# Performance work log

Hardware: AMD Instinct MI355X
Metric: run time of the kernel (lower is better)

## Reference

```python
import jax, jax.numpy as jnp
import numpy as np

B, F, D = 4096, 39, 16          # batch, num_field, embedding_size
V = 1000000                     # num_feat (vocab)
H1, H2 = 128, 128               # cin_layer_sizes
INPUT_DIM = F * D               # 624
FC_DIM = H1 // 2 + H2           # 192 (split_half)
DEEP = [400, 400]
BN_EPS = 1e-5


def setup_inputs() -> dict:
    key = jax.random.key(0)
    ks = jax.random.split(key, 16)
    xav = lambda k, shp: jax.random.normal(k, shp, jnp.float32) * np.sqrt(2.0 / (shp[0] + shp[-1]))
    return {
        "feat_index": jax.random.randint(ks[0], (B, F), 0, V),
        "feat_value": jax.random.uniform(ks[1], (B, F), jnp.float32),
        "emb_table": xav(ks[2], (V, D)),
        "linear_w": xav(ks[3], (INPUT_DIM, 1)),
        "linear_b": jnp.zeros((1,), jnp.float32),
        "conv_w1": xav(ks[4], (H1, F, F)),          # (out, h_prev, m) == conv1d 1x1 weight reshaped
        "conv_b1": jnp.zeros((H1,), jnp.float32),
        "conv_w2": xav(ks[5], (H2, H1 // 2, F)),
        "conv_b2": jnp.zeros((H2,), jnp.float32),
        "deep_w1": xav(ks[6], (INPUT_DIM, DEEP[0])),
        "deep_b1": jnp.zeros((DEEP[0],), jnp.float32),
        "bn_g1": jnp.ones((DEEP[0],), jnp.float32),
        "bn_b1": jnp.zeros((DEEP[0],), jnp.float32),
        "deep_w2": xav(ks[7], (DEEP[0], DEEP[1])),
        "deep_b2": jnp.zeros((DEEP[1],), jnp.float32),
        "bn_g2": jnp.ones((DEEP[1],), jnp.float32),
        "bn_b2": jnpp if False else jnp.zeros((DEEP[1],), jnp.float32),
        "out_w": xav(ks[8], (1 + FC_DIM + DEEP[1], 1)),
        "out_b": jnp.zeros((1,), jnp.float32),
    }


def _bn(x, g, b):
    # torch BatchNorm1d in training mode: biased batch variance
    m = x.mean(axis=0)
    v = x.var(axis=0)
    return g * (x - m) * jax.lax.rsqrt(v + BN_EPS) + b


def reference(feat_index, feat_value, emb_table, linear_w, linear_b,
              conv_w1, conv_b1, conv_w2, conv_b2,
              deep_w1, deep_b1, bn_g1, bn_b1,
              deep_w2, deep_b2, bn_g2, bn_b2,
              out_w, out_b):
    e = emb_table[feat_index]                      # [B, F, D]
    flat = e.reshape(e.shape[0], -1)               # [B, F*D]
    linear_part = flat @ linear_w + linear_b       # [B, 1]

    # CIN: fused outer-product + 1x1 conv (x_k[b,o,d] = sum_{h,m} W[o,h,m] x_prev[b,h,d] x0[b,m,d])
    x0 = e
    h1 = jax.nn.relu(jnp.einsum('bhd,bmd,ohm->bod', x0, x0, conv_w1) + conv_b1[None, :, None])
    nxt, hi1 = jnp.split(h1, 2, axis=1)            # split_half
    h2 = jax.nn.relu(jnp.einsum('bhd,bmd,ohm->bod', nxt, x0, conv_w2) + conv_b2[None, :, None])
    res = jnp.concatenate([hi1, h2], axis=1).sum(axis=2)   # [B, FC_DIM]

    # Deep tower (dropout off / deterministic)
    y = jax.nn.relu(_bn(flat @ deep_w1 + deep_b1, bn_g1, bn_b1))
    y = jax.nn.relu(_bn(y @ deep_w2 + deep_b2, bn_g2, bn_b2))

    cat = jnp.concatenate([linear_part, res, y], axis=1)   # [B, 593]
    return cat @ out_w + out_b
```

## Files before the change

kernel.cpp:

```cpp
#include <hip/hip_runtime.h>

#define BATCH   4096
#define NF      39
#define ED      16
#define IN_DIM  624
#define DW      400
#define BN_EPS  1e-5f
#define NKSG    78
#define AK1     640
#define NKS1    20
#define NKS2    13
#define WCOL    416

typedef __attribute__((ext_vector_type(8))) short short8;
typedef __attribute__((ext_vector_type(4))) float f32x4;
typedef __attribute__((ext_vector_type(2))) float f32x2;
typedef unsigned short u16;

__device__ inline unsigned pack_hi2(float a, float b) {
  return __builtin_amdgcn_perm(__float_as_uint(b), __float_as_uint(a), 0x07060302u);
}
__device__ inline unsigned bf16_rne(float f) {
  unsigned u = __float_as_uint(f);
  u += 0x7fff + ((u >> 16) & 1);
  return u >> 16;
}
__device__ inline float bf2f(u16 v) { return __uint_as_float((unsigned)v << 16); }

#define CIN_E (NKSG * 128 * 32)
#define D1_E  (NKS1 * WCOL * 32)
#define D2_E  (NKS2 * WCOL * 32)
#define PREP_E (CIN_E + D1_E + D2_E + 1600)
#define PREP_B ((PREP_E + 255) / 256)
#define GATH_B (BATCH / 4)

__global__ __launch_bounds__(256) void k_gp(const int* __restrict__ idx,
    const float* __restrict__ emb, const float* __restrict__ lw,
    const float* __restrict__ lb, const float* __restrict__ w1,
    const float* __restrict__ w2, const float* __restrict__ dw1,
    const float* __restrict__ dw2, u16* __restrict__ flatb,
    float* __restrict__ lp, u16* __restrict__ wp1, u16* __restrict__ wp2,
    u16* __restrict__ wpd1, u16* __restrict__ wpd2, float* __restrict__ gstat) {
  int t = threadIdx.x;
  if (blockIdx.x < GATH_B) {
    int lane = t & 63;
    int b = blockIdx.x * 4 + (t >> 6);
    int sj = (lane < NF) ? idx[b * NF + lane] : 0;
    float acc = 0.f;
#pragma unroll
    for (int i = 0; i < 10; i++) {
      int e = lane + i * 64;
      if (e < IN_DIM) {
        int f = e >> 4;
        int row = __shfl(sj, f);
        float v = emb[(size_t)row * ED + (e & 15)];
        flatb[(size_t)b * AK1 + e] = (u16)bf16_rne(v);
        acc = fmaf(v, lw[e], acc);
      } else {
        flatb[(size_t)b * AK1 + e] = 0;
      }
    }
#pragma unroll
    for (int k = 1; k < 64; k <<= 1) acc += __shfl_xor(acc, k);
    if (lane == 0) lp[b] = acc + lb[0];
  } else {
    int e = (blockIdx.x - GATH_B) * 256 + t;
    if (e < CIN_E) {
      int ksg = e >> 12, r = e & 4095, n = r >> 5, kk = r & 31;
      int k = ksg * 32 + kk, h = k & 63, m = k >> 6;
      float v1 = (h < NF) ? w1[(size_t)n * (NF * NF) + h * NF + m] : 0.f;
      float v2 = w2[(size_t)n * (64 * NF) + h * NF + m];
      wp1[e] = (u16)bf16_rne(v1);
      wp2[e] = (u16)bf16_rne(v2);
    } else if (e < CIN_E + D1_E) {
      int e2 = e - CIN_E;
      int ksg = e2 / (WCOL * 32), r = e2 - ksg * (WCOL * 32);
      int col = r >> 5, kk = r & 31;
      int k = ksg * 32 + kk;
      wpd1[e2] = (k < IN_DIM && col < DW) ? (u16)bf16_rne(dw1[(size_t)k * DW + col]) : 0;
    } else if (e < CIN_E + D1_E + D2_E) {
      int e2 = e - CIN_E - D1_E;
      int ksg = e2 / (WCOL * 32), r = e2 - ksg * (WCOL * 32);
      int col = r >> 5, kk = r & 31;
      int k = ksg * 32 + kk;
      wpd2[e2] = (k < DW && col < DW) ? (u16)bf16_rne(dw2[(size_t)k * DW + col]) : 0;
    } else if (e < PREP_E) {
      gstat[e - CIN_E - D1_E - D2_E] = 0.f;
    }
  }
}

template <bool LAY2>
__global__ __launch_bounds__(256, 2) void k_cin_mfma(
    const u16* __restrict__ flatb, const u16* __restrict__ nxtg,
    const u16* __restrict__ wp, const float* __restrict__ bias,
    u16* __restrict__ nxt_out, float* __restrict__ res) {
  int t = threadIdx.x;
  int w = t >> 6, lane = t & 63;
  int nl = lane & 15, q = lane >> 4;
  int d = nl;
  int b0 = blockIdx.x * 16 + w * 4;
  int c0 = blockIdx.y * 64;

  f32x2 nxf[4][2][4];
  if (LAY2) {
#pragma unroll
    for (int si = 0; si < 4; si++)
#pragma unroll
      for (int ks = 0; ks < 2; ks++) {
        uint4 v = *(const uint4*)(nxtg +
            (((size_t)(b0 + si) * 16 + d) * 64 + ks * 32 + q * 8));
        unsigned uu[4] = {v.x, v.y, v.z, v.w};
#pragma unroll
        for (int w4 = 0; w4 < 4; w4++)
          nxf[si][ks][w4] = (f32x2){__uint_as_float(uu[w4] << 16),
                                    __uint_as_float(uu[w4] & 0xffff0000u)};
      }
  } else {
#pragma unroll
    for (int si = 0; si < 4; si++)
#pragma unroll
      for (int ks = 0; ks < 2; ks++)
#pragma unroll
        for (int w4 = 0; w4 < 4; w4++) {
          int h0 = ks * 32 + q * 8 + 2 * w4;
          int h1 = h0 + 1;
          float f0 = (h0 < NF) ? bf2f(flatb[(size_t)(b0 + si) * AK1 + h0 * 16 + d]) : 0.f;
          float f1 = (h1 < NF) ? bf2f(flatb[(size_t)(b0 + si) * AK1 + h1 * 16 + d]) : 0.f;
          nxf[si][ks][w4] = (f32x2){f0, f1};
        }
  }

  f32x4 acc[4][4];
#pragma unroll
  for (int si = 0; si < 4; si++)
#pragma unroll
    for (int nt = 0; nt < 4; nt++) acc[si][nt] = (f32x4){0.f, 0.f, 0.f, 0.f};

  const u16* wbase = wp + (size_t)(c0 + nl) * 32 + q * 8;
  short8 bfr[3][4];
#pragma unroll
  for (int nt = 0; nt < 4; nt++) {
    bfr[0][nt] = *(const short8*)(wbase + nt * 512);
    bfr[1][nt] = *(const short8*)(wbase + 4096 + nt * 512);
  }

  float xv[4], xvn[4];
#pragma unroll
  for (int si = 0; si < 4; si++)
    xv[si] = bf2f(flatb[(size_t)(b0 + si) * AK1 + d]);

  for (int mg = 0; mg < 13; mg++) {
#pragma unroll
    for (int j = 0; j < 6; j++) {
      int ksg = mg * 6 + j;
      int ks = j & 1;
      if (j < 4 || mg < 12) {
        const u16* wb = wbase + (size_t)(ksg + 2) * 4096;
#pragma unroll
        for (int nt = 0; nt < 4; nt++)
          bfr[(j + 2) % 3][nt] = *(const short8*)(wb + nt * 512);
      }
      if (ks == 0) {
        int m = ksg >> 1;
#pragma unroll
        for (int si = 0; si < 4; si++)
          xvn[si] = bf2f(flatb[(size_t)(b0 + si) * AK1 + (m + 1) * 16 + d]);
      }
      short8 afr[4];
#pragma unroll
      for (int si = 0; si < 4; si++) {
        union { unsigned u[4]; short8 s; } a;
        f32x2 xv2 = (f32x2){xv[si], xv[si]};
#pragma unroll
        for (int w4 = 0; w4 < 4; w4++) {
          f32x2 p = nxf[si][ks][w4] * xv2;
          a.u[w4] = pack_hi2(p[0], p[1]);
        }
        afr[si] = a.s;
      }
#pragma unroll
      for (int nt = 0; nt < 4; nt++)
#pragma unroll
        for (int si = 0; si < 4; si++)
          acc[si][nt] = __builtin_amdgcn_mfma_f32_16x16x32_bf16(
              afr[si], bfr[j % 3][nt], acc[si][nt], 0, 0, 0);
      if (ks == 1) {
#pragma unroll
        for (int si = 0; si < 4; si++) xv[si] = xvn[si];
      }
    }
  }

#pragma unroll
  for (int si = 0; si < 4; si++) {
    int b = b0 + si;
#pragma unroll
    for (int nt = 0; nt < 4; nt++) {
      int o = c0 + nt * 16 + nl;
      float bi = bias[o];
      if (!LAY2 && c0 == 0) {
#pragma unroll
        for (int r = 0; r < 4; r++) {
          float v = fmaxf(acc[si][nt][r] + bi, 0.f);
          nxt_out[((size_t)b * 16 + q * 4 + r) * 64 + o] = (u16)bf16_rne(v);
        }
      } else {
        float s = 0.f;
#pragma unroll
        for (int r = 0; r < 4; r++) s += fmaxf(acc[si][nt][r] + bi, 0.f);
        s += __shfl_xor(s, 16);
        s += __shfl_xor(s, 32);
        if (q == 0) {
          int ri = LAY2 ? (64 + o) : (o - 64);
          res[(size_t)b * 192 + ri] = s;
        }
      }
    }
  }
}

template <bool BN_A, int NKS, int KREAL, int AK>
__global__ __launch_bounds__(256) void k_gemm_mfma(
    const u16* __restrict__ Abf, const float* __restrict__ Af32,
    const u16* __restrict__ wp, const float* __restrict__ bias,
    const float* __restrict__ gsIn, const float* __restrict__ gs2In,
    const float* __restrict__ bng, const float* __restrict__ bnb,
    float* __restrict__ C, float* __restrict__ gs, float* __restrict__ gs2) {
  __shared__ float lsS[NKS * 32], lsH[NKS * 32];
  __shared__ float lred[64];
  int t = threadIdx.x;
  if (BN_A) {
    for (int c = t; c < NKS * 32; c += 256) {
      float sc = 0.f, sh = 0.f;
      if (c < DW) {
        float m = gsIn[c] * (1.f / BATCH);
        float var = gs2In[c] * (1.f / BATCH) - m * m;
        sc = bng[c] * rsqrtf(var + BN_EPS);
        sh = bnb[c] - m * sc;
      }
      lsS[c] = sc; lsH[c] = sh;
    }
  }
  if (t < 64) lred[t] = 0.f;
  __syncthreads();

  int w = t >> 6, lane = t & 63;
  int nl = lane & 15, q = lane >> 4;
  int row = blockIdx.x * 64 + w * 16 + nl;
  int c0 = blockIdx.y * 32;
  f32x4 acc[2];
  acc[0] = (f32x4){0.f, 0.f, 0.f, 0.f};
  acc[1] = (f32x4){0.f, 0.f, 0.f, 0.f};

  short8 araw[2]; f32x4 fraw0[2], fraw1[2]; short8 braw[2][2];
  auto loadA_raw = [&](int ksg, int buf) {
    int kb = ksg * 32 + q * 8;
    if (!BN_A) {
      araw[buf] = *(const short8*)(Abf + (size_t)row * AK + kb);
    } else {
      if (kb + 8 <= KREAL) {
        fraw0[buf] = *(const f32x4*)(Af32 + (size_t)row * KREAL + kb);
        fraw1[buf] = *(const f32x4*)(Af32 + (size_t)row * KREAL + kb + 4);
      } else {
        fraw0[buf] = (f32x4){0.f,0.f,0.f,0.f};
        fraw1[buf] = (f32x4){0.f,0.f,0.f,0.f};
      }
    }
    const u16* wb = wp + (size_t)ksg * (WCOL * 32) + (size_t)(c0 + nl) * 32 + q * 8;
    braw[buf][0] = *(const short8*)wb;
    braw[buf][1] = *(const short8*)(wb + 16 * 32);
  };
  auto cookA = [&](int ksg, int buf) -> short8 {
    if (!BN_A) return araw[buf];
    int kb = ksg * 32 + q * 8;
    f32x4 s0 = *(const f32x4*)&lsS[kb], h0 = *(const f32x4*)&lsH[kb];
    f32x4 s1 = *(const f32x4*)&lsS[kb + 4], h1 = *(const f32x4*)&lsH[kb + 4];
    union { unsigned u[4]; short8 s; } a;
    float v0 = fmaxf(fmaf(fraw0[buf][0], s0[0], h0[0]), 0.f);
    float v1 = fmaxf(fmaf(fraw0[buf][1], s0[1], h0[1]), 0.f);
    float v2 = fmaxf(fmaf(fraw0[buf][2], s0[2], h0[2]), 0.f);
    float v3 = fmaxf(fmaf(fraw0[buf][3], s0[3], h0[3]), 0.f);
    float v4 = fmaxf(fmaf(fraw1[buf][0], s1[0], h1[0]), 0.f);
    float v5 = fmaxf(fmaf(fraw1[buf][1], s1[1], h1[1]), 0.f);
    float v6 = fmaxf(fmaf(fraw1[buf][2], s1[2], h1[2]), 0.f);
    float v7 = fmaxf(fmaf(fraw1[buf][3], s1[3], h1[3]), 0.f);
    a.u[0] = bf16_rne(v0) | (bf16_rne(v1) << 16);
    a.u[1] = bf16_rne(v2) | (bf16_rne(v3) << 16);
    a.u[2] = bf16_rne(v4) | (bf16_rne(v5) << 16);
    a.u[3] = bf16_rne(v6) | (bf16_rne(v7) << 16);
    return a.s;
  };

  loadA_raw(0, 0);
#pragma unroll 4
  for (int ksg = 0; ksg < NKS; ksg++) {
    int cur = ksg & 1;
    if (ksg + 1 < NKS) loadA_raw(ksg + 1, cur ^ 1);
    short8 afr = cookA(ksg, cur);
    acc[0] = __builtin_amdgcn_mfma_f32_16x16x32_bf16(afr, braw[cur][0], acc[0], 0, 0, 0);
    acc[1] = __builtin_amdgcn_mfma_f32_16x16x32_bf16(afr, braw[cur][1], acc[1], 0, 0, 0);
  }

  int rbase = blockIdx.x * 64 + w * 16 + q * 4;
#pragma unroll
  for (int nt = 0; nt < 2; nt++) {
    int col = c0 + nt * 16 + nl;
    if (col < DW) {
      float bi = bias[col];
      float s = 0.f, s2 = 0.f;
#pragma unroll
      for (int r = 0; r < 4; r++) {
        float v = acc[nt][r] + bi;
        C[(size_t)(rbase + r) * DW + col] = v;
        s += v; s2 = fmaf(v, v, s2);
      }
      s += __shfl_xor(s, 16); s2 += __shfl_xor(s2, 16);
      s += __shfl_xor(s, 32); s2 += __shfl_xor(s2, 32);
      if (q == 0) {
        atomicAdd(&lred[nt * 16 + nl], s);
        atomicAdd(&lred[32 + nt * 16 + nl], s2);
      }
    }
  }
  __syncthreads();
  if (t < 32) {
    int col = c0 + t;
    if (col < DW) atomicAdd(&gs[col], lred[t]);
  } else if (t < 64) {
    int col = c0 + t - 32;
    if (col < DW) atomicAdd(&gs2[col], lred[t]);
  }
}

__global__ __launch_bounds__(256) void k_final(const float* __restrict__ lp,
    const float* __restrict__ res, const float* __restrict__ y2,
    const float* __restrict__ gB, const float* __restrict__ gB2,
    const float* __restrict__ g2, const float* __restrict__ bb2,
    const float* __restrict__ ow, const float* __restrict__ ob,
    float* __restrict__ out) {
  __shared__ float lsS[DW], lsH[DW];
  int t = threadIdx.x;
  for (int c = t; c < DW; c += 256) {
    float m = gB[c] * (1.f / BATCH);
    float var = gB2[c] * (1.f / BATCH) - m * m;
    float sc = g2[c] * rsqrtf(var + BN_EPS);
    lsS[c] = sc;
    lsH[c] = bb2[c] - m * sc;
  }
  __syncthreads();
  int lane = t & 63, w = t >> 6;
  int b = blockIdx.x * 4 + w;
  float acc = 0.f;
  for (int j = lane; j < 593; j += 64) {
    float v;
    if (j == 0)       v = lp[b];
    else if (j < 193) v = res[(size_t)b * 192 + (j - 1)];
    else {
      int c = j - 193;
      v = fmaxf(fmaf(y2[(size_t)b * DW + c], lsS[c], lsH[c]), 0.f);
    }
    acc = fmaf(v, ow[j], acc);
  }
#pragma unroll
  for (int k = 1; k < 64; k <<= 1) acc += __shfl_xor(acc, k);
  if (lane == 0) out[b] = acc + ob[0];
}

extern "C" void kernel_launch(void* const* d_in, const int* in_sizes, int n_in,
                              void* d_out, int out_size, void* d_ws, size_t ws_size,
                              hipStream_t stream) {
  const int*   feat_index = (const int*)d_in[0];
  const float* emb = (const float*)d_in[2];
  const float* lw  = (const float*)d_in[3];
  const float* lb  = (const float*)d_in[4];
  const float* w1  = (const float*)d_in[5];
  const float* b1  = (const float*)d_in[6];
  const float* w2  = (const float*)d_in[7];
  const float* b2  = (const float*)d_in[8];
  const float* dw1 = (const float*)d_in[9];
  const float* db1 = (const float*)d_in[10];
  const float* g1  = (const float*)d_in[11];
  const float* bb1 = (const float*)d_in[12];
  const float* dw2 = (const float*)d_in[13];
  const float* db2 = (const float*)d_in[14];
  const float* g2  = (const float*)d_in[15];
  const float* bb2 = (const float*)d_in[16];
  const float* ow  = (const float*)d_in[17];
  const float* ob  = (const float*)d_in[18];

  float* ws   = (float*)d_ws;
  u16*  flatb = (u16*)ws;
  float* y1   = ws + 1310720;
  float* res  = ws + 2949120;
  float* lp   = ws + 3735552;
  float* gA   = ws + 3741248;
  float* gA2  = gA + 400;
  float* gB   = gA2 + 400;
  float* gB2  = gB + 400;
  u16*  nxtg  = (u16*)(ws + 3742848);
  float* y2   = ws + 3742848;
  u16*  wp1   = (u16*)(ws + 5840000);
  u16*  wp2   = (u16*)(ws + 6003840);
  u16*  wpd1  = (u16*)(ws + 6167680);
  u16*  wpd2  = (u16*)(ws + 6300800);
  float* out  = (float*)d_out;

  k_gp<<<GATH_B + PREP_B, 256, 0, stream>>>(feat_index, emb, lw, lb, w1, w2,
      dw1, dw2, flatb, lp, wp1, wp2, wpd1, wpd2, gA);
  k_cin_mfma<false><<<dim3(BATCH / 16, 2), 256, 0, stream>>>(
      flatb, nullptr, wp1, b1, nxtg, res);
  k_cin_mfma<true><<<dim3(BATCH / 16, 2), 256, 0, stream>>>(
      flatb, nxtg, wp2, b2, nullptr, res);
  k_gemm_mfma<false, NKS1, IN_DIM, AK1><<<dim3(BATCH / 64, 13), 256, 0, stream>>>(
      flatb, nullptr, wpd1, db1, nullptr, nullptr, nullptr, nullptr, y1, gA, gA2);
  k_gemm_mfma<true, NKS2, DW, 0><<<dim3(BATCH / 64, 13), 256, 0, stream>>>(
      nullptr, y1, wpd2, db2, gA, gA2, g1, bb1, y2, gB, gB2);
  k_final<<<BATCH / 4, 256, 0, stream>>>(lp, res, y2, gB, gB2, g2, bb2, ow, ob, out);
}
```

Measured before the change: 270.6 us.

## Co-schedule CIN layers with deep-tower GEMMs in fused heterogeneous kernels

Merges each CIN layer launch with the matching deep-tower GEMM launch into one grid. Even blocks below 1024 run CIN tiles, and the remaining blocks run GEMM tiles, so the two independent workloads overlap on the GPU and two launches plus their tail bubbles go away. This only runs when the workspace is large enough, because y2 must be relocated so it does not alias nxtg while both run together; the weight-pack offsets are also shifted. The fused kernel takes the CIN launch bounds (256, 2), which may constrain registers for the GEMM path.

```diff
diff --git a/kernel.cpp b/kernel.cpp
--- a/kernel.cpp
+++ b/kernel.cpp
@@ -91,16 +91,15 @@
 }
 
 template <bool LAY2>
-__global__ __launch_bounds__(256, 2) void k_cin_mfma(
+__device__ __forceinline__ void cin_body(int cidx, int t,
     const u16* __restrict__ flatb, const u16* __restrict__ nxtg,
     const u16* __restrict__ wp, const float* __restrict__ bias,
     u16* __restrict__ nxt_out, float* __restrict__ res) {
-  int t = threadIdx.x;
   int w = t >> 6, lane = t & 63;
   int nl = lane & 15, q = lane >> 4;
   int d = nl;
-  int b0 = blockIdx.x * 16 + w * 4;
-  int c0 = blockIdx.y * 64;
+  int b0 = (cidx >> 1) * 16 + w * 4;
+  int c0 = (cidx & 1) * 64;
 
   f32x2 nxf[4][2][4];
   if (LAY2) {
@@ -221,15 +220,13 @@
 }
 
 template <bool BN_A, int NKS, int KREAL, int AK>
-__global__ __launch_bounds__(256) void k_gemm_mfma(
+__device__ __forceinline__ void gemm_body(int gx, int gy, int t,
+    float* lsS, float* lsH, float* lred,
     const u16* __restrict__ Abf, const float* __restrict__ Af32,
     const u16* __restrict__ wp, const float* __restrict__ bias,
     const float* __restrict__ gsIn, const float* __restrict__ gs2In,
     const float* __restrict__ bng, const float* __restrict__ bnb,
     float* __restrict__ C, float* __restrict__ gs, float* __restrict__ gs2) {
-  __shared__ float lsS[NKS * 32], lsH[NKS * 32];
-  __shared__ float lred[64];
-  int t = threadIdx.x;
   if (BN_A) {
     for (int c = t; c < NKS * 32; c += 256) {
       float sc = 0.f, sh = 0.f;
@@ -247,8 +244,8 @@
 
   int w = t >> 6, lane = t & 63;
   int nl = lane & 15, q = lane >> 4;
-  int row = blockIdx.x * 64 + w * 16 + nl;
-  int c0 = blockIdx.y * 32;
+  int row = gx * 64 + w * 16 + nl;
+  int c0 = gy * 32;
   f32x4 acc[2];
   acc[0] = (f32x4){0.f, 0.f, 0.f, 0.f};
   acc[1] = (f32x4){0.f, 0.f, 0.f, 0.f};
@@ -302,7 +299,7 @@
     acc[1] = __builtin_amdgcn_mfma_f32_16x16x32_bf16(afr, braw[cur][1], acc[1], 0, 0, 0);
   }
 
-  int rbase = blockIdx.x * 64 + w * 16 + q * 4;
+  int rbase = gx * 64 + w * 16 + q * 4;
 #pragma unroll
   for (int nt = 0; nt < 2; nt++) {
     int col = c0 + nt * 16 + nl;
@@ -331,6 +328,68 @@
     int col = c0 + t - 32;
     if (col < DW) atomicAdd(&gs2[col], lred[t]);
   }
+}
+
+template <bool PH2>
+__device__ __forceinline__ void gemm_go(int gx, int gy, int t,
+    float* lsS, float* lsH, float* lred,
+    const u16* Abf, const float* Af32, const u16* wpd, const float* dbias,
+    const float* gsIn, const float* gs2In, const float* bng, const float* bnb,
+    float* C, float* gs, float* gs2) {
+  if (PH2)
+    gemm_body<true, NKS2, DW, 0>(gx, gy, t, lsS, lsH, lred, Abf, Af32, wpd,
+        dbias, gsIn, gs2In, bng, bnb, C, gs, gs2);
+  else
+    gemm_body<false, NKS1, IN_DIM, AK1>(gx, gy, t, lsS, lsH, lred, Abf, Af32,
+        wpd, dbias, gsIn, gs2In, bng, bnb, C, gs, gs2);
+}
+
+template <bool PH2>
+__global__ __launch_bounds__(256, 2) void k_fused(
+    const u16* __restrict__ flatb, const u16* __restrict__ nxtg,
+    const u16* __restrict__ wpc, const float* __restrict__ cbias,
+    u16* __restrict__ nxt_out, float* __restrict__ res,
+    const u16* __restrict__ Abf, const float* __restrict__ Af32,
+    const u16* __restrict__ wpd, const float* __restrict__ dbias,
+    const float* __restrict__ gsIn, const float* __restrict__ gs2In,
+    const float* __restrict__ bng, const float* __restrict__ bnb,
+    float* __restrict__ C, float* __restrict__ gs, float* __restrict__ gs2) {
+  __shared__ float lsS[640], lsH[640], lred[64];
+  int bid = blockIdx.x;
+  int t = threadIdx.x;
+  if (bid < 1024) {
+    if (!(bid & 1)) {
+      cin_body<PH2>(bid >> 1, t, flatb, nxtg, wpc, cbias, nxt_out, res);
+      return;
+    }
+    gemm_go<PH2>((bid >> 1) & 63, (bid >> 1) >> 6, t, lsS, lsH, lred,
+                 Abf, Af32, wpd, dbias, gsIn, gs2In, bng, bnb, C, gs, gs2);
+  } else {
+    int g = bid - 512;
+    gemm_go<PH2>(g & 63, g >> 6, t, lsS, lsH, lred,
+                 Abf, Af32, wpd, dbias, gsIn, gs2In, bng, bnb, C, gs, gs2);
+  }
+}
+
+template <bool LAY2>
+__global__ __launch_bounds__(256, 2) void k_cin_mfma(
+    const u16* __restrict__ flatb, const u16* __restrict__ nxtg,
+    const u16* __restrict__ wp, const float* __restrict__ bias,
+    u16* __restrict__ nxt_out, float* __restrict__ res) {
+  cin_body<LAY2>(blockIdx.x * 2 + blockIdx.y, threadIdx.x, flatb, nxtg, wp,
+                 bias, nxt_out, res);
+}
+
+template <bool PH2>
+__global__ __launch_bounds__(256) void k_gemm_mfma(
+    const u16* __restrict__ Abf, const float* __restrict__ Af32,
+    const u16* __restrict__ wp, const float* __restrict__ bias,
+    const float* __restrict__ gsIn, const float* __restrict__ gs2In,
+    const float* __restrict__ bng, const float* __restrict__ bnb,
+    float* __restrict__ C, float* __restrict__ gs, float* __restrict__ gs2) {
+  __shared__ float lsS[640], lsH[640], lred[64];
+  gemm_go<PH2>(blockIdx.x, blockIdx.y, threadIdx.x, lsS, lsH, lred,
+               Abf, Af32, wp, bias, gsIn, gs2In, bng, bnb, C, gs, gs2);
 }
 
 __global__ __launch_bounds__(256) void k_final(const float* __restrict__ lp,
@@ -399,22 +458,36 @@
   float* gB   = gA2 + 400;
   float* gB2  = gB + 400;
   u16*  nxtg  = (u16*)(ws + 3742848);
-  float* y2   = ws + 3742848;
   u16*  wp1   = (u16*)(ws + 5840000);
-  u16*  wp2   = (u16*)(ws + 6003840);
-  u16*  wpd1  = (u16*)(ws + 6167680);
-  u16*  wpd2  = (u16*)(ws + 6300800);
+  u16*  wp2   = (u16*)(ws + 5999744);
+  u16*  wpd1  = (u16*)(ws + 6159488);
+  u16*  wpd2  = (u16*)(ws + 6292608);
   float* out  = (float*)d_out;
+
+  bool bigws = ws_size >= (size_t)8017536 * 4;
+  float* y2  = bigws ? (ws + 6379136) : (ws + 3742848);
 
   k_gp<<<GATH_B + PREP_B, 256, 0, stream>>>(feat_index, emb, lw, lb, w1, w2,
       dw1, dw2, flatb, lp, wp1, wp2, wpd1, wpd2, gA);
-  k_cin_mfma<false><<<dim3(BATCH / 16, 2), 256, 0, stream>>>(
-      flatb, nullptr, wp1, b1, nxtg, res);
-  k_cin_mfma<true><<<dim3(BATCH / 16, 2), 256, 0, stream>>>(
-      flatb, nxtg, wp2, b2, nullptr, res);
-  k_gemm_mfma<false, NKS1, IN_DIM, AK1><<<dim3(BATCH / 64, 13), 256, 0, stream>>>(
-      flatb, nullptr, wpd1, db1, nullptr, nullptr, nullptr, nullptr, y1, gA, gA2);
-  k_gemm_mfma<true, NKS2, DW, 0><<<dim3(BATCH / 64, 13), 256, 0, stream>>>(
-      nullptr, y1, wpd2, db2, gA, gA2, g1, bb1, y2, gB, gB2);
+  if (bigws) {
+    k_fused<false><<<1344, 256, 0, stream>>>(
+        flatb, nullptr, wp1, b1, nxtg, res,
+        flatb, nullptr, wpd1, db1, nullptr, nullptr, nullptr, nullptr,
+        y1, gA, gA2);
+    k_fused<true><<<1344, 256, 0, stream>>>(
+        flatb, nxtg, wp2, b2, nullptr, res,
+        nullptr, y1, wpd2, db2, gA, gA2, g1, bb1,
+        y2, gB, gB2);
+  } else {
+    k_cin_mfma<false><<<dim3(BATCH / 16, 2), 256, 0, stream>>>(
+        flatb, nullptr, wp1, b1, nxtg, res);
+    k_cin_mfma<true><<<dim3(BATCH / 16, 2), 256, 0, stream>>>(
+        flatb, nxtg, wp2, b2, nullptr, res);
+    k_gemm_mfma<false><<<dim3(BATCH / 64, 13), 256, 0, stream>>>(
+        flatb, nullptr, wpd1, db1, nullptr, nullptr, nullptr, nullptr,
+        y1, gA, gA2);
+    k_gemm_mfma<true><<<dim3(BATCH / 64, 13), 256, 0, stream>>>(
+        nullptr, y1, wpd2, db2, gA, gA2, g1, bb1, y2, gB, gB2);
+  }
   k_final<<<BATCH / 4, 256, 0, stream>>>(lp, res, y2, gB, gB2, g2, bb2, ow, ob, out);
 }
```

Result: slower. 335.8 us (+24.1%).

## Rewrite CIN kernels to use 32x32x16 MFMA with full output columns per block

Applied to the files above, without the earlier changes.

The CIN layers move from 16x16x32 bf16 MFMA tiles, where each wave handled 4 batch rows against 64 output channels, to 32x32x16 MFMA tiles. In the new layout each wave covers 2 batch rows times 16 dims as the M dimension and all 128 output channels. The weight pre-packing switches to k-steps of 16 to match, and the grid drops the channel split, so the outer-product A fragments are built once per wave instead of twice across blocks. The goal is to remove the redundant A-fragment construction and get more work per MFMA instruction. The cost is larger accumulators and a more intricate output index mapping.

```diff
diff --git a/kernel.cpp b/kernel.cpp
--- a/kernel.cpp
+++ b/kernel.cpp
@@ -6,13 +6,14 @@
 #define IN_DIM  624
 #define DW      400
 #define BN_EPS  1e-5f
-#define NKSG    78
+#define NK16    156
 #define AK1     640
 #define NKS1    20
 #define NKS2    13
 #define WCOL    416
 
 typedef __attribute__((ext_vector_type(8))) short short8;
+typedef __attribute__((ext_vector_type(16))) float f32x16;
 typedef __attribute__((ext_vector_type(4))) float f32x4;
 typedef __attribute__((ext_vector_type(2))) float f32x2;
 typedef unsigned short u16;
@@ -27,7 +28,7 @@
 }
 __device__ inline float bf2f(u16 v) { return __uint_as_float((unsigned)v << 16); }
 
-#define CIN_E (NKSG * 128 * 32)
+#define CIN_E (NK16 * 128 * 16)
 #define D1_E  (NKS1 * WCOL * 32)
 #define D2_E  (NKS2 * WCOL * 32)
 #define PREP_E (CIN_E + D1_E + D2_E + 1600)
@@ -66,10 +67,10 @@
   } else {
     int e = (blockIdx.x - GATH_B) * 256 + t;
     if (e < CIN_E) {
-      int ksg = e >> 12, r = e & 4095, n = r >> 5, kk = r & 31;
-      int k = ksg * 32 + kk, h = k & 63, m = k >> 6;
-      float v1 = (h < NF) ? w1[(size_t)n * (NF * NF) + h * NF + m] : 0.f;
-      float v2 = w2[(size_t)n * (64 * NF) + h * NF + m];
+      int k16 = e >> 11, r = e & 2047, col = r >> 4, kk = r & 15;
+      int k = k16 * 16 + kk, h = k & 63, m = k >> 6;
+      float v1 = (h < NF) ? w1[(size_t)col * (NF * NF) + h * NF + m] : 0.f;
+      float v2 = w2[(size_t)col * (64 * NF) + h * NF + m];
       wp1[e] = (u16)bf16_rne(v1);
       wp2[e] = (u16)bf16_rne(v2);
     } else if (e < CIN_E + D1_E) {
@@ -91,130 +92,113 @@
 }
 
 template <bool LAY2>
-__global__ __launch_bounds__(256, 2) void k_cin_mfma(
+__global__ __launch_bounds__(256, 2) void k_cin32(
     const u16* __restrict__ flatb, const u16* __restrict__ nxtg,
     const u16* __restrict__ wp, const float* __restrict__ bias,
     u16* __restrict__ nxt_out, float* __restrict__ res) {
   int t = threadIdx.x;
   int w = t >> 6, lane = t & 63;
-  int nl = lane & 15, q = lane >> 4;
-  int d = nl;
-  int b0 = blockIdx.x * 16 + w * 4;
-  int c0 = blockIdx.y * 64;
-
-  f32x2 nxf[4][2][4];
+  int col = lane & 31, khalf = lane >> 5;
+  int si = (lane >> 4) & 1, d = lane & 15;
+  int b0 = blockIdx.x * 8 + w * 2;
+  int b = b0 + si;
+  const u16* fb = flatb + (size_t)b * AK1;
+
+  f32x2 sp[4][4];
   if (LAY2) {
 #pragma unroll
-    for (int si = 0; si < 4; si++)
-#pragma unroll
-      for (int ks = 0; ks < 2; ks++) {
-        uint4 v = *(const uint4*)(nxtg +
-            (((size_t)(b0 + si) * 16 + d) * 64 + ks * 32 + q * 8));
-        unsigned uu[4] = {v.x, v.y, v.z, v.w};
-#pragma unroll
-        for (int w4 = 0; w4 < 4; w4++)
-          nxf[si][ks][w4] = (f32x2){__uint_as_float(uu[w4] << 16),
-                                    __uint_as_float(uu[w4] & 0xffff0000u)};
-      }
+    for (int s = 0; s < 4; s++) {
+      uint4 v = *(const uint4*)(nxtg + (((size_t)b * 16 + d) * 64 + s * 16 + khalf * 8));
+      unsigned uu[4] = {v.x, v.y, v.z, v.w};
+#pragma unroll
+      for (int w4 = 0; w4 < 4; w4++)
+        sp[s][w4] = (f32x2){__uint_as_float(uu[w4] << 16),
+                            __uint_as_float(uu[w4] & 0xffff0000u)};
+    }
   } else {
 #pragma unroll
-    for (int si = 0; si < 4; si++)
-#pragma unroll
-      for (int ks = 0; ks < 2; ks++)
-#pragma unroll
-        for (int w4 = 0; w4 < 4; w4++) {
-          int h0 = ks * 32 + q * 8 + 2 * w4;
-          int h1 = h0 + 1;
-          float f0 = (h0 < NF) ? bf2f(flatb[(size_t)(b0 + si) * AK1 + h0 * 16 + d]) : 0.f;
-          float f1 = (h1 < NF) ? bf2f(flatb[(size_t)(b0 + si) * AK1 + h1 * 16 + d]) : 0.f;
-          nxf[si][ks][w4] = (f32x2){f0, f1};
-        }
-  }
-
-  f32x4 acc[4][4];
-#pragma unroll
-  for (int si = 0; si < 4; si++)
-#pragma unroll
-    for (int nt = 0; nt < 4; nt++) acc[si][nt] = (f32x4){0.f, 0.f, 0.f, 0.f};
-
-  const u16* wbase = wp + (size_t)(c0 + nl) * 32 + q * 8;
+    for (int s = 0; s < 4; s++)
+#pragma unroll
+      for (int w4 = 0; w4 < 4; w4++) {
+        int h0 = s * 16 + khalf * 8 + 2 * w4;
+        int h1 = h0 + 1;
+        float f0 = (h0 < NF) ? bf2f(fb[h0 * 16 + d]) : 0.f;
+        float f1 = (h1 < NF) ? bf2f(fb[h1 * 16 + d]) : 0.f;
+        sp[s][w4] = (f32x2){f0, f1};
+      }
+  }
+
+  f32x16 acc[4];
+#pragma unroll
+  for (int nt = 0; nt < 4; nt++)
+#pragma unroll
+    for (int r = 0; r < 16; r++) acc[nt][r] = 0.f;
+
+  const u16* wbase = wp + (size_t)col * 16 + khalf * 8;
   short8 bfr[3][4];
 #pragma unroll
   for (int nt = 0; nt < 4; nt++) {
     bfr[0][nt] = *(const short8*)(wbase + nt * 512);
-    bfr[1][nt] = *(const short8*)(wbase + 4096 + nt * 512);
-  }
-
-  float xv[4], xvn[4];
-#pragma unroll
-  for (int si = 0; si < 4; si++)
-    xv[si] = bf2f(flatb[(size_t)(b0 + si) * AK1 + d]);
+    bfr[1][nt] = *(const short8*)(wbase + 2048 + nt * 512);
+  }
+
+  float xv = bf2f(fb[d]);
+  float xvn;
 
   for (int mg = 0; mg < 13; mg++) {
 #pragma unroll
-    for (int j = 0; j < 6; j++) {
-      int ksg = mg * 6 + j;
-      int ks = j & 1;
-      if (j < 4 || mg < 12) {
-        const u16* wb = wbase + (size_t)(ksg + 2) * 4096;
+    for (int j = 0; j < 12; j++) {
+      int k16 = mg * 12 + j;
+      if (j == 0 || j == 4 || j == 8) {
+        int mn = mg * 3 + (j >> 2) + 1;
+        xvn = bf2f(fb[mn * 16 + d]);
+      }
+      if (j < 10 || mg < 12) {
+        const u16* wb = wbase + (size_t)(k16 + 2) * 2048;
 #pragma unroll
         for (int nt = 0; nt < 4; nt++)
           bfr[(j + 2) % 3][nt] = *(const short8*)(wb + nt * 512);
       }
-      if (ks == 0) {
-        int m = ksg >> 1;
-#pragma unroll
-        for (int si = 0; si < 4; si++)
-          xvn[si] = bf2f(flatb[(size_t)(b0 + si) * AK1 + (m + 1) * 16 + d]);
-      }
-      short8 afr[4];
-#pragma unroll
-      for (int si = 0; si < 4; si++) {
-        union { unsigned u[4]; short8 s; } a;
-        f32x2 xv2 = (f32x2){xv[si], xv[si]};
-#pragma unroll
-        for (int w4 = 0; w4 < 4; w4++) {
-          f32x2 p = nxf[si][ks][w4] * xv2;
-          a.u[w4] = pack_hi2(p[0], p[1]);
-        }
-        afr[si] = a.s;
+      int s = j & 3;
+      union { unsigned u[4]; short8 v; } a;
+      f32x2 xv2 = (f32x2){xv, xv};
+#pragma unroll
+      for (int w4 = 0; w4 < 4; w4++) {
+        f32x2 p = sp[s][w4] * xv2;
+        a.u[w4] = pack_hi2(p[0], p[1]);
       }
 #pragma unroll
       for (int nt = 0; nt < 4; nt++)
-#pragma unroll
-        for (int si = 0; si < 4; si++)
-          acc[si][nt] = __builtin_amdgcn_mfma_f32_16x16x32_bf16(
-              afr[si], bfr[j % 3][nt], acc[si][nt], 0, 0, 0);
-      if (ks == 1) {
-#pragma unroll
-        for (int si = 0; si < 4; si++) xv[si] = xvn[si];
-      }
-    }
-  }
-
-#pragma unroll
-  for (int si = 0; si < 4; si++) {
-    int b = b0 + si;
-#pragma unroll
-    for (int nt = 0; nt < 4; nt++) {
-      int o = c0 + nt * 16 + nl;
-      float bi = bias[o];
-      if (!LAY2 && c0 == 0) {
-#pragma unroll
-        for (int r = 0; r < 4; r++) {
-          float v = fmaxf(acc[si][nt][r] + bi, 0.f);
-          nxt_out[((size_t)b * 16 + q * 4 + r) * 64 + o] = (u16)bf16_rne(v);
-        }
-      } else {
-        float s = 0.f;
-#pragma unroll
-        for (int r = 0; r < 4; r++) s += fmaxf(acc[si][nt][r] + bi, 0.f);
-        s += __shfl_xor(s, 16);
-        s += __shfl_xor(s, 32);
-        if (q == 0) {
-          int ri = LAY2 ? (64 + o) : (o - 64);
-          res[(size_t)b * 192 + ri] = s;
-        }
+        acc[nt] = __builtin_amdgcn_mfma_f32_32x32x16_bf16(
+            a.v, bfr[j % 3][nt], acc[nt], 0, 0, 0);
+      if (s == 3) xv = xvn;
+    }
+  }
+
+#pragma unroll
+  for (int nt = 0; nt < 4; nt++) {
+    int o = nt * 32 + col;
+    float bi = bias[o];
+    if (!LAY2 && nt < 2) {
+#pragma unroll
+      for (int r = 0; r < 16; r++) {
+        int si2 = r >> 3;
+        int dd = (r & 3) + 8 * ((r >> 2) & 1) + 4 * khalf;
+        float v = fmaxf(acc[nt][r] + bi, 0.f);
+        nxt_out[((size_t)(b0 + si2) * 16 + dd) * 64 + o] = (u16)bf16_rne(v);
+      }
+    } else {
+      float p0 = 0.f, p1 = 0.f;
+#pragma unroll
+      for (int r = 0; r < 8; r++)  p0 += fmaxf(acc[nt][r] + bi, 0.f);
+#pragma unroll
+      for (int r = 8; r < 16; r++) p1 += fmaxf(acc[nt][r] + bi, 0.f);
+      p0 += __shfl_xor(p0, 32);
+      p1 += __shfl_xor(p1, 32);
+      if (khalf == 0) {
+        int ri = LAY2 ? (64 + o) : (o - 64);
+        res[(size_t)b0 * 192 + ri] = p0;
+        res[(size_t)(b0 + 1) * 192 + ri] = p1;
       }
     }
   }
@@ -401,17 +385,15 @@
   u16*  nxtg  = (u16*)(ws + 3742848);
   float* y2   = ws + 3742848;
   u16*  wp1   = (u16*)(ws + 5840000);
-  u16*  wp2   = (u16*)(ws + 6003840);
-  u16*  wpd1  = (u16*)(ws + 6167680);
-  u16*  wpd2  = (u16*)(ws + 6300800);
+  u16*  wp2   = (u16*)(ws + 5999744);
+  u16*  wpd1  = (u16*)(ws + 6159488);
+  u16*  wpd2  = (u16*)(ws + 6292608);
   float* out  = (float*)d_out;
 
   k_gp<<<GATH_B + PREP_B, 256, 0, stream>>>(feat_index, emb, lw, lb, w1, w2,
       dw1, dw2, flatb, lp, wp1, wp2, wpd1, wpd2, gA);
-  k_cin_mfma<false><<<dim3(BATCH / 16, 2), 256, 0, stream>>>(
-      flatb, nullptr, wp1, b1, nxtg, res);
-  k_cin_mfma<true><<<dim3(BATCH / 16, 2), 256, 0, stream>>>(
-      flatb, nxtg, wp2, b2, nullptr, res);
+  k_cin32<false><<<512, 256, 0, stream>>>(flatb, nullptr, wp1, b1, nxtg, res);
+  k_cin32<true><<<512, 256, 0, stream>>>(flatb, nxtg, wp2, b2, nullptr, res);
   k_gemm_mfma<false, NKS1, IN_DIM, AK1><<<dim3(BATCH / 64, 13), 256, 0, stream>>>(
       flatb, nullptr, wpd1, db1, nullptr, nullptr, nullptr, nullptr, y1, gA, gA2);
   k_gemm_mfma<true, NKS2, DW, 0><<<dim3(BATCH / 64, 13), 256, 0, stream>>>(
```

After: 269.4 us. No clear change (-0.4%).
